# Optimization experiments

Measured on AMD Instinct MI355X. Metric: run time of the kernel, lower is better.

The kernel has to match this reference:

```python
import jax, jax.numpy as jnp
import numpy as np

BS, SEQ, DIM, NH = 2, 2048, 2048, 16
HD = DIM // NH  # 128


def setup_inputs() -> dict:
    key = jax.random.key(0)
    ks = jax.random.split(key, 6)
    x = jax.random.normal(ks[0], (BS, SEQ, DIM), dtype=jnp.float32)
    # rotary frequencies, theta=10000 as in LLaMA
    inv_freq = 1.0 / (10000.0 ** (jnp.arange(0, HD, 2, dtype=jnp.float32) / HD))  # [HD/2]
    t = jnp.arange(SEQ, dtype=jnp.float32)
    freqs = jnp.outer(t, inv_freq)  # [SEQ, HD/2]
    freqs_cos = jnp.cos(freqs)
    freqs_sin = jnp.sin(freqs)
    # additive causal mask [1,1,S,S]
    causal = jnp.tril(jnp.ones((SEQ, SEQ), dtype=bool))
    mask = jnp.where(causal, 0.0, -1e9).astype(jnp.float32)[None, None]
    scale = 0.02
    wq = jax.random.normal(ks[1], (DIM, DIM), dtype=jnp.float32) * scale
    wk = jax.random.normal(ks[2], (DIM, DIM), dtype=jnp.float32) * scale
    wv = jax.random.normal(ks[3], (DIM, DIM), dtype=jnp.float32) * scale
    wo = jax.random.normal(ks[4], (DIM, DIM), dtype=jnp.float32) * scale
    return {"x": x, "freqs_cos": freqs_cos, "freqs_sin": freqs_sin, "mask": mask,
            "wq": wq, "wk": wk, "wv": wv, "wo": wo}


def _apply_rope(t, cos, sin):
    # t: [b,s,h,hd]; cos/sin: [s,hd/2]
    tr = t.reshape(*t.shape[:-1], HD // 2, 2)
    tre, tim = tr[..., 0], tr[..., 1]
    c = cos[None, :, None, :]
    s = sin[None, :, None, :]
    out_re = tre * c - tim * s
    out_im = tre * s + tim * c
    return jnp.stack([out_re, out_im], axis=-1).reshape(t.shape)


def reference(x, freqs_cos, freqs_sin, mask, wq, wk, wv, wo):
    bs, seq, _ = x.shape
    q = (x @ wq).reshape(bs, seq, NH, HD)
    k = (x @ wk).reshape(bs, seq, NH, HD)
    v = (x @ wv).reshape(bs, seq, NH, HD)
    q = _apply_rope(q, freqs_cos, freqs_sin)
    k = _apply_rope(k, freqs_cos, freqs_sin)
    # [b,h,s,s]
    scores = jnp.einsum("bqhd,bkhd->bhqk", q, k) / np.sqrt(HD).astype(np.float32)
    scores = scores + mask
    probs = jax.nn.softmax(scores, axis=-1)
    out = jnp.einsum("bhqk,bkhd->bqhd", probs, v).reshape(bs, seq, DIM)
    return out @ wo
```

## Files before the change

kernel.cpp:

```cpp
#include <hip/hip_runtime.h>
#include <hip/hip_bf16.h>
#include <stdint.h>
#include <stddef.h>

#define SEQ 2048
#define DIM 2048
#define NH 16
#define HD 128
#define BSZ 2
#define MTOT (BSZ*SEQ)
#define KDIM 2048
#define NT_K (KDIM/64)

typedef __bf16 bf16;
typedef __attribute__((ext_vector_type(4))) __bf16 bf16x4;
typedef __attribute__((ext_vector_type(8))) __bf16 bf16x8;
typedef __attribute__((ext_vector_type(4))) float f32x4;

#define MFMA16(a,b,c) __builtin_amdgcn_mfma_f32_16x16x32_bf16((a),(b),(c),0,0,0)

__device__ __forceinline__ void glds16(const void* g, void* l) {
  __builtin_amdgcn_global_load_lds((__attribute__((address_space(1))) void*)(g),
                                   (__attribute__((address_space(3))) void*)(l),
                                   16, 0, 0);
}

__device__ __forceinline__ f32x4 f4zero() { f32x4 v = {0.f, 0.f, 0.f, 0.f}; return v; }

__device__ __forceinline__ uint32_t bpack(float a, float b) {
  uint16_t au = __builtin_bit_cast(uint16_t, (bf16)a);
  uint16_t bu = __builtin_bit_cast(uint16_t, (bf16)b);
  return (uint32_t)au | ((uint32_t)bu << 16);
}

__global__ void cast_x_bf16(const float* __restrict__ in, bf16* __restrict__ out) {
  size_t i = (size_t)blockIdx.x * blockDim.x + threadIdx.x;
  float4 v = ((const float4*)in)[i];
  bf16x4 ov;
  ov.x = (bf16)v.x; ov.y = (bf16)v.y; ov.z = (bf16)v.z; ov.w = (bf16)v.w;
  ((bf16x4*)out)[i] = ov;
}

__global__ void transpose_w(const float* __restrict__ W, bf16* __restrict__ WT) {
  __shared__ float tile[64][65];
  const int bk = blockIdx.x, bn = blockIdx.y;
  const int tid = threadIdx.x;
  const int tc = tid & 15, tr = tid >> 4;
#pragma unroll
  for (int p = 0; p < 4; ++p) {
    int k = tr + p * 16;
    float4 v = *(const float4*)(W + (size_t)(bk * 64 + k) * DIM + bn * 64 + tc * 4);
    tile[k][tc * 4 + 0] = v.x;
    tile[k][tc * 4 + 1] = v.y;
    tile[k][tc * 4 + 2] = v.z;
    tile[k][tc * 4 + 3] = v.w;
  }
  __syncthreads();
#pragma unroll
  for (int p = 0; p < 4; ++p) {
    int n = tr + p * 16;
    bf16x4 ov;
    ov.x = (bf16)tile[tc * 4 + 0][n];
    ov.y = (bf16)tile[tc * 4 + 1][n];
    ov.z = (bf16)tile[tc * 4 + 2][n];
    ov.w = (bf16)tile[tc * 4 + 3][n];
    *(bf16x4*)(WT + (size_t)(bn * 64 + n) * DIM + bk * 64 + tc * 4) = ov;
  }
}

template<int MODE>
__global__ __launch_bounds__(512, 2)
void gemm8(const bf16* __restrict__ A, const bf16* __restrict__ BT,
           float* __restrict__ out0,
           bf16* __restrict__ qb, bf16* __restrict__ kbuf, bf16* __restrict__ vT,
           const float* __restrict__ cosT, const float* __restrict__ sinT)
{
  extern __shared__ uint8_t smem[];
  const int tid = threadIdx.x;
  const int lane = tid & 63, w = tid >> 6;
  const int l15 = lane & 15, h4 = lane >> 4;
  const int wr = w & 3, wc = w >> 2;

  const int f = blockIdx.x;
  const int cpx = gridDim.x >> 3;
  const int swz = (f & 7) * cpx + (f >> 3);
  const int bm = swz & 15;
  const int bn = swz >> 4;

  const size_t strideB = (size_t)KDIM * 2;
  const uint8_t* Ab = (const uint8_t*)A + (size_t)(bm * 256) * strideB;
  const uint8_t* Bb = (const uint8_t*)BT + (size_t)(bn * 128) * strideB;

  auto stage = [&](int buf, int t) {
    uint8_t* la = smem + buf * 49152;
    uint8_t* lb = la + 32768;
    const int kb0 = t * 128;
#pragma unroll
    for (int i = 0; i < 4; ++i) {
      int chunk = i * 512 + tid;
      int row = chunk >> 3, c = chunk & 7;
      int cs = c ^ (row & 7);
      glds16(Ab + (size_t)row * strideB + kb0 + cs * 16, la + chunk * 16);
    }
#pragma unroll
    for (int i = 0; i < 2; ++i) {
      int chunk = i * 512 + tid;
      int row = chunk >> 3, c = chunk & 7;
      int cs = c ^ (row & 7);
      glds16(Bb + (size_t)row * strideB + kb0 + cs * 16, lb + chunk * 16);
    }
  };

  f32x4 acc[4][4];
#pragma unroll
  for (int m = 0; m < 4; ++m)
#pragma unroll
    for (int n = 0; n < 4; ++n) acc[m][n] = f4zero();

  stage(0, 0);
  stage(1, 1);

#pragma unroll 1
  for (int t = 0; t < NT_K; ++t) {
    if (t < NT_K - 1) { asm volatile("s_waitcnt vmcnt(6)" ::: "memory"); }
    else              { asm volatile("s_waitcnt vmcnt(0)" ::: "memory"); }
    __builtin_amdgcn_s_barrier();
    asm volatile("" ::: "memory");

    const uint8_t* la = smem + (t & 1) * 49152;
    const uint8_t* lb = la + 32768;
    bf16x8 aF[4][2], bF[4][2];
#pragma unroll
    for (int m = 0; m < 4; ++m) {
      int row = wr * 64 + m * 16 + l15;
#pragma unroll
      for (int ks = 0; ks < 2; ++ks)
        aF[m][ks] = *(const bf16x8*)(la + row * 128 + (((ks * 4 + h4) ^ (row & 7)) * 16));
    }
#pragma unroll
    for (int n = 0; n < 4; ++n) {
      int row = wc * 64 + n * 16 + l15;
#pragma unroll
      for (int ks = 0; ks < 2; ++ks)
        bF[n][ks] = *(const bf16x8*)(lb + row * 128 + (((ks * 4 + h4) ^ (row & 7)) * 16));
    }
    __builtin_amdgcn_s_setprio(1);
#pragma unroll
    for (int ks = 0; ks < 2; ++ks)
#pragma unroll
      for (int m = 0; m < 4; ++m)
#pragma unroll
        for (int n = 0; n < 4; ++n)
          acc[m][n] = MFMA16(aF[m][ks], bF[n][ks], acc[m][n]);
    __builtin_amdgcn_s_setprio(0);

    asm volatile("" ::: "memory");
    __builtin_amdgcn_s_barrier();
    asm volatile("" ::: "memory");
    if (t + 2 < NT_K) stage(t & 1, t + 2);
  }

  const int row0 = bm * 256 + wr * 64;
  const int col0 = bn * 128 + wc * 64;
#pragma unroll
  for (int m = 0; m < 4; ++m) {
#pragma unroll
    for (int n = 0; n < 4; ++n) {
#pragma unroll
      for (int r = 0; r < 4; ++r) {
        int row = row0 + m * 16 + h4 * 4 + r;
        int col = col0 + n * 16 + l15;
        float v = acc[m][n][r];
        if constexpr (MODE == 0) {
          out0[(size_t)row * DIM + col] = v;
        } else {
          int seg = col >> 11;
          int ccol = col & (DIM - 1);
          if (seg < 2) {
            float v2 = __shfl_xor(v, 1);
            int s = row & (SEQ - 1);
            int jidx = (ccol & (HD - 1)) >> 1;
            float c = cosT[s * (HD / 2) + jidx];
            float sn = sinT[s * (HD / 2) + jidx];
            float o = (col & 1) ? fmaf(v2, sn, v * c) : fmaf(v, c, -(v2 * sn));
            bf16* dst = (seg == 0) ? qb : kbuf;
            dst[(size_t)row * DIM + ccol] = (bf16)o;
          } else {
            int hh = ccol >> 7, d = ccol & (HD - 1);
            int bb = row >> 11, s = row & (SEQ - 1);
            vT[((size_t)(bb * NH + hh) * HD + d) * SEQ + s] = (bf16)v;
          }
        }
      }
    }
  }
}

__global__ __launch_bounds__(256, 2)
void flash_attn(const bf16* __restrict__ Q, const bf16* __restrict__ Kg,
                const bf16* __restrict__ VT, bf16* __restrict__ O)
{
  __shared__ __align__(16) bf16 Ks[2][64 * 128];
  __shared__ __align__(16) bf16 Vs[2][128 * 64];

  const int fidx = blockIdx.x;
  const int xr = fidx & 7, inner = fidx >> 3;
  const int pr = inner & 15;
  const int g = xr + 8 * (inner >> 4);
  const int h = g & 15, b = g >> 4;

  const int tid = threadIdx.x, lane = tid & 63, w = tid >> 6;
  const int l15 = lane & 15, h4 = lane >> 4;
  const bool hhalf = ((h4 >> 1) & 1) != 0;

  const float scale = 0.08838834764831845f;
  const uint8_t* kgb = (const uint8_t*)Kg + ((size_t)(b * SEQ) * DIM + h * HD) * 2;
  const uint8_t* vgb = (const uint8_t*)VT + ((size_t)(b * NH + h) * HD * SEQ) * 2;

  auto stageKV = [&](int buf, int t) {
    const uint8_t* ksrc = kgb + (size_t)t * 64 * (DIM * 2);
    const uint8_t* vsrc = vgb + (size_t)t * 64 * 2;
#pragma unroll
    for (int j = 0; j < 4; ++j) {
      int chunk = w * 256 + j * 64 + lane;
      int key = chunk >> 4, ck = chunk & 15;
      int jk = (ck * 16) ^ ((key & 7) << 4);
      glds16(ksrc + (size_t)key * (DIM * 2) + jk,
             (uint8_t*)&Ks[buf][0] + (w * 256 + j * 64) * 16);
      int d = chunk >> 3, cv = chunk & 7;
      int jv = (cv * 16) ^ ((d & 7) << 4);
      glds16(vsrc + (size_t)d * (SEQ * 2) + jv,
             (uint8_t*)&Vs[buf][0] + (w * 256 + j * 64) * 16);
    }
  };

#pragma unroll 1
  for (int qsel = 0; qsel < 2; ++qsel) {
    const int qt = qsel ? (SEQ / 64 - 1 - pr) : pr;
    const int q0 = qt * 64;
    const int qrow = q0 + w * 16 + l15;

    const bf16* qbase = Q + ((size_t)(b * SEQ + qrow)) * DIM + h * HD;
    bf16x8 aQ[4];
#pragma unroll
    for (int kk = 0; kk < 4; ++kk)
      aQ[kk] = *(const bf16x8*)(qbase + kk * 32 + h4 * 8);

    f32x4 o[8];
#pragma unroll
    for (int i = 0; i < 8; ++i) o[i] = f4zero();
    float mrun = -1e30f, lrun = 0.0f;

    stageKV(0, 0);
    __syncthreads();

#pragma unroll 1
    for (int t = 0; t <= qt; ++t) {
      const int cur = t & 1;
      if (t < qt) stageKV(cur ^ 1, t + 1);

      f32x4 S[4];
      __builtin_amdgcn_s_setprio(1);
#pragma unroll
      for (int kb = 0; kb < 4; ++kb) {
        f32x4 a = f4zero();
        int key = kb * 16 + l15;
        int swzk = (key & 7) << 4;
#pragma unroll
        for (int kk = 0; kk < 4; ++kk) {
          bf16x8 aK = *(const bf16x8*)((const uint8_t*)&Ks[cur][0] + key * 256 +
                                       (((kk * 32 + h4 * 8) * 2) ^ swzk));
          a = MFMA16(aK, aQ[kk], a);
        }
        S[kb] = a;
      }
      __builtin_amdgcn_s_setprio(0);

      if (t == qt) {
#pragma unroll
        for (int kb = 0; kb < 4; ++kb)
#pragma unroll
          for (int r = 0; r < 4; ++r) {
            int key = q0 + kb * 16 + h4 * 4 + r;
            float sv = S[kb][r] * scale;
            S[kb][r] = (key > qrow) ? -1e9f : sv;
          }
      } else {
#pragma unroll
        for (int kb = 0; kb < 4; ++kb)
#pragma unroll
          for (int r = 0; r < 4; ++r) S[kb][r] *= scale;
      }

      float pmax = S[0][0];
#pragma unroll
      for (int kb = 0; kb < 4; ++kb)
#pragma unroll
        for (int r = 0; r < 4; ++r) pmax = fmaxf(pmax, S[kb][r]);
      pmax = fmaxf(pmax, __shfl_xor(pmax, 16));
      pmax = fmaxf(pmax, __shfl_xor(pmax, 32));
      float mnew = fmaxf(mrun, pmax);
      float corr = __expf(mrun - mnew);
      float p[4][4];
      float psum = 0.f;
#pragma unroll
      for (int kb = 0; kb < 4; ++kb)
#pragma unroll
        for (int r = 0; r < 4; ++r) {
          float pv = __expf(S[kb][r] - mnew);
          p[kb][r] = pv;
          psum += pv;
        }
      psum += __shfl_xor(psum, 16);
      psum += __shfl_xor(psum, 32);
      lrun = lrun * corr + psum;
      mrun = mnew;
#pragma unroll
      for (int i = 0; i < 8; ++i) o[i] *= corr;

      uint32_t pk[4][2];
#pragma unroll
      for (int kb = 0; kb < 4; ++kb) {
        pk[kb][0] = bpack(p[kb][0], p[kb][1]);
        pk[kb][1] = bpack(p[kb][2], p[kb][3]);
      }

      bf16x8 pB[2];
#pragma unroll
      for (int kb2 = 0; kb2 < 2; ++kb2) {
        uint32_t s0a = hhalf ? pk[kb2 * 2 + 1][0] : pk[kb2 * 2][0];
        uint32_t s0b = hhalf ? pk[kb2 * 2 + 1][1] : pk[kb2 * 2][1];
        uint32_t s1a = hhalf ? pk[kb2 * 2][0] : pk[kb2 * 2 + 1][0];
        uint32_t s1b = hhalf ? pk[kb2 * 2][1] : pk[kb2 * 2 + 1][1];
        uint32_t e16a = __shfl_xor(s0a, 16), e16b = __shfl_xor(s0b, 16);
        uint32_t e32a = __shfl_xor(s1a, 32), e32b = __shfl_xor(s1b, 32);
        uint32_t e48a = __shfl_xor(s1a, 48), e48b = __shfl_xor(s1b, 48);
        uint32_t lo0 = (h4 == 0) ? s0a : (h4 == 1) ? e48a : (h4 == 2) ? e32a : e16a;
        uint32_t lo1 = (h4 == 0) ? s0b : (h4 == 1) ? e48b : (h4 == 2) ? e32b : e16b;
        uint32_t hi0 = (h4 == 0) ? e16a : (h4 == 1) ? e32a : (h4 == 2) ? e48a : s0a;
        uint32_t hi1 = (h4 == 0) ? e16b : (h4 == 1) ? e32b : (h4 == 2) ? e48b : s0b;
        uint4 u = make_uint4(lo0, lo1, hi0, hi1);
        pB[kb2] = __builtin_bit_cast(bf16x8, u);
      }

      __builtin_amdgcn_s_setprio(1);
#pragma unroll
      for (int db = 0; db < 8; ++db) {
        int drow = db * 16 + l15;
        int swzv = (drow & 7) << 4;
#pragma unroll
        for (int kb2 = 0; kb2 < 2; ++kb2) {
          bf16x8 aV = *(const bf16x8*)((const uint8_t*)&Vs[cur][0] + drow * 128 +
                                       (((kb2 * 32 + h4 * 8) * 2) ^ swzv));
          o[db] = MFMA16(aV, pB[kb2], o[db]);
        }
      }
      __builtin_amdgcn_s_setprio(0);

      __syncthreads();
    }

    float inv = 1.0f / lrun;
    bf16* obase = O + ((size_t)(b * SEQ + qrow)) * DIM + h * HD;
#pragma unroll
    for (int db = 0; db < 8; ++db) {
      uint32_t w0 = bpack(o[db][0] * inv, o[db][1] * inv);
      uint32_t w1 = bpack(o[db][2] * inv, o[db][3] * inv);
      uint2 st = make_uint2(w0, w1);
      *(uint2*)(obase + db * 16 + h4 * 4) = st;
    }
  }
}

extern "C" void kernel_launch(void* const* d_in, const int* in_sizes, int n_in,
                              void* d_out, int out_size, void* d_ws, size_t ws_size,
                              hipStream_t stream)
{
  const float* x    = (const float*)d_in[0];
  const float* fcos = (const float*)d_in[1];
  const float* fsin = (const float*)d_in[2];
  const float* wq   = (const float*)d_in[4];
  const float* wk   = (const float*)d_in[5];
  const float* wv   = (const float*)d_in[6];
  const float* wo   = (const float*)d_in[7];

  uint8_t* ws = (uint8_t*)d_ws;
  const size_t SZ_XB = (size_t)MTOT * DIM * 2;
  const size_t SZ_WT = (size_t)DIM * DIM * 2;

  bf16* xb    = (bf16*)(ws);
  bf16* wqT   = (bf16*)(ws + SZ_XB);
  bf16* wkT   = (bf16*)(ws + SZ_XB + 1 * SZ_WT);
  bf16* wvT   = (bf16*)(ws + SZ_XB + 2 * SZ_WT);
  bf16* woT   = (bf16*)(ws + SZ_XB + 3 * SZ_WT);
  bf16* qb    = (bf16*)(ws + SZ_XB + 4 * SZ_WT);
  bf16* kb    = (bf16*)(ws + 2 * SZ_XB + 4 * SZ_WT);
  bf16* vT    = (bf16*)(ws + 3 * SZ_XB + 4 * SZ_WT);
  bf16* attnb = xb;

  hipFuncSetAttribute((const void*)gemm8<1>,
                      hipFuncAttributeMaxDynamicSharedMemorySize, 98304);
  hipFuncSetAttribute((const void*)gemm8<0>,
                      hipFuncAttributeMaxDynamicSharedMemorySize, 98304);

  cast_x_bf16<<<(MTOT * DIM) / (256 * 4), 256, 0, stream>>>(x, xb);
  dim3 tg(DIM / 64, DIM / 64);
  transpose_w<<<tg, 256, 0, stream>>>(wq, wqT);
  transpose_w<<<tg, 256, 0, stream>>>(wk, wkT);
  transpose_w<<<tg, 256, 0, stream>>>(wv, wvT);
  transpose_w<<<tg, 256, 0, stream>>>(wo, woT);

  gemm8<1><<<768, 512, 98304, stream>>>(xb, wqT, nullptr, qb, kb, vT, fcos, fsin);

  flash_attn<<<512, 256, 0, stream>>>(qb, kb, vT, attnb);

  gemm8<0><<<256, 512, 98304, stream>>>(attnb, woT, (float*)d_out,
                                        nullptr, nullptr, nullptr, nullptr, nullptr);
}
```

Baseline: 434.6 us.

## Restructure GEMM into four-slot BK=32 pipeline with early fragment loads

```diff
diff --git a/kernel.cpp b/kernel.cpp
--- a/kernel.cpp
+++ b/kernel.cpp
@@ -10,7 +10,7 @@
 #define BSZ 2
 #define MTOT (BSZ*SEQ)
 #define KDIM 2048
-#define NT_K (KDIM/64)
+#define NTL (KDIM/32)
 
 typedef __bf16 bf16;
 typedef __attribute__((ext_vector_type(4))) __bf16 bf16x4;
@@ -70,7 +70,7 @@
 
 template<int MODE>
 __global__ __launch_bounds__(512, 2)
-void gemm8(const bf16* __restrict__ A, const bf16* __restrict__ BT,
+void gemm9(const bf16* __restrict__ A, const bf16* __restrict__ BT,
            float* __restrict__ out0,
            bf16* __restrict__ qb, bf16* __restrict__ kbuf, bf16* __restrict__ vT,
            const float* __restrict__ cosT, const float* __restrict__ sinT)
@@ -91,24 +91,21 @@
   const uint8_t* Ab = (const uint8_t*)A + (size_t)(bm * 256) * strideB;
   const uint8_t* Bb = (const uint8_t*)BT + (size_t)(bn * 128) * strideB;
 
-  auto stage = [&](int buf, int t) {
-    uint8_t* la = smem + buf * 49152;
-    uint8_t* lb = la + 32768;
-    const int kb0 = t * 128;
-#pragma unroll
-    for (int i = 0; i < 4; ++i) {
-      int chunk = i * 512 + tid;
-      int row = chunk >> 3, c = chunk & 7;
-      int cs = c ^ (row & 7);
-      glds16(Ab + (size_t)row * strideB + kb0 + cs * 16, la + chunk * 16);
-    }
-#pragma unroll
-    for (int i = 0; i < 2; ++i) {
-      int chunk = i * 512 + tid;
-      int row = chunk >> 3, c = chunk & 7;
-      int cs = c ^ (row & 7);
-      glds16(Bb + (size_t)row * strideB + kb0 + cs * 16, lb + chunk * 16);
-    }
+  const int r0 = tid >> 2;
+  const int g0 = tid & 3;
+
+  auto stage = [&](int t) {
+    uint8_t* slot = smem + (t & 3) * 24576;
+    const int k0 = t * 64;
+    int row = r0;
+    glds16(Ab + (size_t)row * strideB + k0 + ((g0 ^ ((row >> 1) & 3)) << 4),
+           slot + tid * 16);
+    row = 128 + r0;
+    glds16(Ab + (size_t)row * strideB + k0 + ((g0 ^ ((row >> 1) & 3)) << 4),
+           slot + 8192 + tid * 16);
+    row = r0;
+    glds16(Bb + (size_t)row * strideB + k0 + ((g0 ^ ((row >> 1) & 3)) << 4),
+           slot + 16384 + tid * 16);
   };
 
   f32x4 acc[4][4];
@@ -117,60 +114,59 @@
 #pragma unroll
     for (int n = 0; n < 4; ++n) acc[m][n] = f4zero();
 
-  stage(0, 0);
-  stage(1, 1);
+  stage(0); stage(1); stage(2);
+  asm volatile("s_waitcnt vmcnt(6)" ::: "memory");
+  __builtin_amdgcn_s_barrier();
+  asm volatile("" ::: "memory");
 
 #pragma unroll 1
-  for (int t = 0; t < NT_K; ++t) {
-    if (t < NT_K - 1) { asm volatile("s_waitcnt vmcnt(6)" ::: "memory"); }
-    else              { asm volatile("s_waitcnt vmcnt(0)" ::: "memory"); }
-    __builtin_amdgcn_s_barrier();
-    asm volatile("" ::: "memory");
-
-    const uint8_t* la = smem + (t & 1) * 49152;
-    const uint8_t* lb = la + 32768;
-    bf16x8 aF[4][2], bF[4][2];
-#pragma unroll
-    for (int m = 0; m < 4; ++m) {
-      int row = wr * 64 + m * 16 + l15;
-#pragma unroll
-      for (int ks = 0; ks < 2; ++ks)
-        aF[m][ks] = *(const bf16x8*)(la + row * 128 + (((ks * 4 + h4) ^ (row & 7)) * 16));
-    }
-#pragma unroll
-    for (int n = 0; n < 4; ++n) {
-      int row = wc * 64 + n * 16 + l15;
-#pragma unroll
-      for (int ks = 0; ks < 2; ++ks)
-        bF[n][ks] = *(const bf16x8*)(lb + row * 128 + (((ks * 4 + h4) ^ (row & 7)) * 16));
-    }
-    __builtin_amdgcn_s_setprio(1);
-#pragma unroll
-    for (int ks = 0; ks < 2; ++ks)
-#pragma unroll
-      for (int m = 0; m < 4; ++m)
-#pragma unroll
-        for (int n = 0; n < 4; ++n)
-          acc[m][n] = MFMA16(aF[m][ks], bF[n][ks], acc[m][n]);
-    __builtin_amdgcn_s_setprio(0);
+  for (int p = 0; p < NTL; ++p) {
+    const uint8_t* sa = smem + (p & 3) * 24576;
+    const uint8_t* sb = sa + 16384;
+    bf16x8 aF[4], bF[4];
+#pragma unroll
+    for (int mf = 0; mf < 4; ++mf) {
+      int row = wr * 64 + mf * 16 + l15;
+      aF[mf] = *(const bf16x8*)(sa + row * 64 + ((h4 ^ ((row >> 1) & 3)) << 4));
+    }
+#pragma unroll
+    for (int nf = 0; nf < 4; ++nf) {
+      int row = wc * 64 + nf * 16 + l15;
+      bF[nf] = *(const bf16x8*)(sb + row * 64 + ((h4 ^ ((row >> 1) & 3)) << 4));
+    }
+    if (p + 3 < NTL) stage(p + 3);
 
     asm volatile("" ::: "memory");
     __builtin_amdgcn_s_barrier();
     asm volatile("" ::: "memory");
-    if (t + 2 < NT_K) stage(t & 1, t + 2);
+
+    __builtin_amdgcn_s_setprio(1);
+#pragma unroll
+    for (int mf = 0; mf < 4; ++mf)
+#pragma unroll
+      for (int nf = 0; nf < 4; ++nf)
+        acc[mf][nf] = MFMA16(aF[mf], bF[nf], acc[mf][nf]);
+    __builtin_amdgcn_s_setprio(0);
+
+    if (p < NTL - 3)       { asm volatile("s_waitcnt vmcnt(6)" ::: "memory"); }
+    else if (p == NTL - 3) { asm volatile("s_waitcnt vmcnt(3)" ::: "memory"); }
+    else if (p == NTL - 2) { asm volatile("s_waitcnt vmcnt(0)" ::: "memory"); }
+    asm volatile("" ::: "memory");
+    __builtin_amdgcn_s_barrier();
+    asm volatile("" ::: "memory");
   }
 
   const int row0 = bm * 256 + wr * 64;
   const int col0 = bn * 128 + wc * 64;
 #pragma unroll
-  for (int m = 0; m < 4; ++m) {
-#pragma unroll
-    for (int n = 0; n < 4; ++n) {
+  for (int mf = 0; mf < 4; ++mf) {
+#pragma unroll
+    for (int nf = 0; nf < 4; ++nf) {
 #pragma unroll
       for (int r = 0; r < 4; ++r) {
-        int row = row0 + m * 16 + h4 * 4 + r;
-        int col = col0 + n * 16 + l15;
-        float v = acc[m][n][r];
+        int row = row0 + mf * 16 + h4 * 4 + r;
+        int col = col0 + nf * 16 + l15;
+        float v = acc[mf][nf][r];
         if constexpr (MODE == 0) {
           out0[(size_t)row * DIM + col] = v;
         } else {
@@ -398,9 +394,9 @@
   bf16* vT    = (bf16*)(ws + 3 * SZ_XB + 4 * SZ_WT);
   bf16* attnb = xb;
 
-  hipFuncSetAttribute((const void*)gemm8<1>,
+  hipFuncSetAttribute((const void*)gemm9<1>,
                       hipFuncAttributeMaxDynamicSharedMemorySize, 98304);
-  hipFuncSetAttribute((const void*)gemm8<0>,
+  hipFuncSetAttribute((const void*)gemm9<0>,
                       hipFuncAttributeMaxDynamicSharedMemorySize, 98304);
 
   cast_x_bf16<<<(MTOT * DIM) / (256 * 4), 256, 0, stream>>>(x, xb);
@@ -410,10 +406,10 @@
   transpose_w<<<tg, 256, 0, stream>>>(wv, wvT);
   transpose_w<<<tg, 256, 0, stream>>>(wo, woT);
 
-  gemm8<1><<<768, 512, 98304, stream>>>(xb, wqT, nullptr, qb, kb, vT, fcos, fsin);
+  gemm9<1><<<768, 512, 98304, stream>>>(xb, wqT, nullptr, qb, kb, vT, fcos, fsin);
 
   flash_attn<<<512, 256, 0, stream>>>(qb, kb, vT, attnb);
 
-  gemm8<0><<<256, 512, 98304, stream>>>(attnb, woT, (float*)d_out,
+  gemm9<0><<<256, 512, 98304, stream>>>(attnb, woT, (float*)d_out,
                                         nullptr, nullptr, nullptr, nullptr, nullptr);
 }
```

New measurement: 427.9 us. About the same (-1.5%).
